# Performance work log

Measured on AMD Instinct MI355X. Metric: run time of the kernel, lower is better.

Reference implementation:

```python
import jax, jax.numpy as jnp
import numpy as np

NUM_HEADS = 8
ROPE_BASE = 10000.0


def _rope_cache(T, D, dtype=jnp.float32):
    # LLaMA-style rope cache: cos/sin of shape [T, D]
    inv_freq = 1.0 / (ROPE_BASE ** (jnp.arange(0, D, 2, dtype=dtype) / D))
    t = jnp.arange(T, dtype=dtype)
    freqs = t[:, None] * inv_freq[None, :]            # [T, D/2]
    emb = jnp.concatenate([freqs, freqs], axis=-1)    # [T, D]
    return jnp.cos(emb), jnp.sin(emb)


def _rotate_half(x):
    x1, x2 = jnp.split(x, 2, axis=-1)
    return jnp.concatenate([-x2, x1], axis=-1)


def setup_inputs() -> dict:
    key = jax.random.key(0)
    k1, k2, k3 = jax.random.split(key, 3)
    B, T, C = 4, 2048, 512
    x = jax.random.normal(k1, (B, T, C), dtype=jnp.float32)
    Wqkv = jax.random.normal(k2, (C, 3 * C), dtype=jnp.float32) * (1.0 / np.sqrt(C))
    Wproj = jax.random.normal(k3, (C, C), dtype=jnp.float32) * (1.0 / np.sqrt(C))
    return {"x": x, "Wqkv": Wqkv, "Wproj": Wproj}


def reference(x, Wqkv, Wproj):
    B, T, C = x.shape
    H = NUM_HEADS
    D = C // H

    qkv = jnp.einsum('btc,cf->btf', x, Wqkv)          # [B,T,3C]
    qkv = qkv.reshape(B, T, H, 3 * D)
    q, k, v = jnp.split(qkv, 3, axis=-1)              # each [B,T,H,D]
    q = q.transpose(0, 2, 1, 3)                       # [B,H,T,D]
    k = k.transpose(0, 2, 1, 3)
    v = v.transpose(0, 2, 1, 3)

    cos, sin = _rope_cache(T, D, dtype=x.dtype)       # [T,D]
    cos = cos[None, None, :, :]
    sin = sin[None, None, :, :]
    q = q * cos + _rotate_half(q) * sin
    k = k * cos + _rotate_half(k) * sin

    scale = 1.0 / np.sqrt(D)
    scores = jnp.einsum('bhqd,bhkd->bhqk', q, k) * scale  # [B,H,T,T]
    causal = jnp.tril(jnp.ones((T, T), dtype=bool))
    scores = jnp.where(causal[None, None, :, :], scores, jnp.finfo(scores.dtype).min)
    attn = jax.nn.softmax(scores, axis=-1)
    out = jnp.einsum('bhqk,bhkd->bhqd', attn, v)      # [B,H,T,D]
    out = out.transpose(0, 2, 1, 3).reshape(B, T, C)
    return jnp.einsum('btc,cd->btd', out, Wproj)
```

## Files before the change

### kernel.cpp

```cpp
#include <hip/hip_runtime.h>
#include <hip/hip_bf16.h>
#include <stdint.h>

constexpr int Bn = 4;
constexpr int Tn = 2048;
constexpr int Cn = 512;
constexpr int Hn = 8;
constexpr int Dn = 64;
constexpr int BT = Bn * Tn;
constexpr int NQKV = 3 * Cn;

typedef __attribute__((ext_vector_type(4))) float  f32x4;
typedef __attribute__((ext_vector_type(8))) short  s16x8;
typedef __attribute__((ext_vector_type(4))) short  s16x4;

__device__ __forceinline__ short f2bs(float f) {
    __hip_bfloat16 h = __float2bfloat16(f);
    return *reinterpret_cast<short*>(&h);
}

__device__ __forceinline__ void gload16(const short* g, short* l) {
    __builtin_amdgcn_global_load_lds(
        (const __attribute__((address_space(1))) void*)g,
        (__attribute__((address_space(3))) void*)l, 16, 0, 0);
}


__global__ __launch_bounds__(256) void k_prep(const float* __restrict__ x,
                                              const float* __restrict__ Wqkv,
                                              const float* __restrict__ Wproj,
                                              short* __restrict__ xb,
                                              short* __restrict__ wqkvT,
                                              short* __restrict__ wprojT,
                                              float2* __restrict__ csT) {
    const int bid = blockIdx.x;
    const int tid = threadIdx.x;
    __shared__ float lds[64 * 65];

    if (bid < 4096) {
        int i = bid * 256 + tid;
        f32x4 v = reinterpret_cast<const f32x4*>(x)[i];
        s16x4 o;
        o[0] = f2bs(v[0]); o[1] = f2bs(v[1]); o[2] = f2bs(v[2]); o[3] = f2bs(v[3]);
        reinterpret_cast<s16x4*>(xb)[i] = o;
    } else if (bid < 4352) {
        int wb = bid - 4096;
        const float* W; short* out; int N, n0, k0;
        if (wb < 192) {
            W = Wqkv; out = wqkvT; N = NQKV;
            n0 = (wb >> 3) * 64; k0 = (wb & 7) * 64;
        } else {
            wb -= 192;
            W = Wproj; out = wprojT; N = Cn;
            n0 = (wb >> 3) * 64; k0 = (wb & 7) * 64;
        }
#pragma unroll
        for (int i = 0; i < 16; ++i) {
            int flat = i * 256 + tid;
            int k = flat >> 6, n = flat & 63;
            lds[n * 65 + k] = W[(size_t)(k0 + k) * N + n0 + n];
        }
        __syncthreads();
#pragma unroll
        for (int i = 0; i < 16; ++i) {
            int flat = i * 256 + tid;
            int n = flat >> 6, k = flat & 63;
            out[(size_t)(n0 + n) * 512 + k0 + k] = f2bs(lds[n * 65 + k]);
        }
    } else {
        int i = (bid - 4352) * 256 + tid;
        int t = i >> 6, d = i & 63;
        float inv = exp2f(-(float)(d & 31) * 0.41524101186f);
        float fr = (float)t * inv;
        csT[i] = make_float2(cosf(fr), sinf(fr));
    }
}


template <int MODE>
__global__ __launch_bounds__(256, 4) void gemm_kernel(
    const short* __restrict__ A, const short* __restrict__ Bt,
    const float2* __restrict__ csT,
    short* __restrict__ Qb, short* __restrict__ Kb, short* __restrict__ Vt,
    float* __restrict__ outF) {
    const int m0 = blockIdx.y * 128;
    const int n0 = blockIdx.x * 128;
    const int tid = threadIdx.x;
    const int w = tid >> 6, lane = tid & 63;
    const int qi = lane & 15, g = lane >> 4;
    const int wr = w >> 1, wc = w & 1;

    __shared__ short As[2][128 * 32];
    __shared__ short Bs[2][128 * 32];

    f32x4 acc[4][4];
#pragma unroll
    for (int mt = 0; mt < 4; ++mt)
#pragma unroll
        for (int nt = 0; nt < 4; ++nt) acc[mt][nt] = (f32x4){0.f, 0.f, 0.f, 0.f};

    const int lrr = lane >> 2;
    const int lp = lane & 3;

#define STAGEG(buf, k0)                                                         \
    {                                                                           \
        _Pragma("unroll")                                                       \
        for (int i_ = 0; i_ < 2; ++i_) {                                        \
            int row_ = i_ * 64 + w * 16 + lrr;                                  \
            int c_ = lp ^ ((row_ ^ (row_ >> 2)) & 3);                           \
            gload16(&A[(size_t)(m0 + row_) * 512 + (k0) + c_ * 8],              \
                    &As[buf][(i_ * 64 + w * 16) * 32 + lane * 8]);              \
            gload16(&Bt[(size_t)(n0 + row_) * 512 + (k0) + c_ * 8],             \
                    &Bs[buf][(i_ * 64 + w * 16) * 32 + lane * 8]);              \
        }                                                                       \
    }

    STAGEG(0, 0);

    for (int it = 0; it < 16; ++it) {
        const int cur = it & 1;
        if (it + 1 < 16) {
            STAGEG((it + 1) & 1, (it + 1) * 32);
            asm volatile("s_waitcnt vmcnt(4)" ::: "memory");
        } else {
            asm volatile("s_waitcnt vmcnt(0)" ::: "memory");
        }
        __builtin_amdgcn_s_barrier();
        asm volatile("" ::: "memory");

        s16x8 af[4], bf[4];
#pragma unroll
        for (int mt = 0; mt < 4; ++mt) {
            int row = wr * 64 + mt * 16 + qi;
            int p = g ^ ((row ^ (row >> 2)) & 3);
            af[mt] = *(const s16x8*)&As[cur][row * 32 + p * 8];
        }
#pragma unroll
        for (int nt = 0; nt < 4; ++nt) {
            int row = wc * 64 + nt * 16 + qi;
            int p = g ^ ((row ^ (row >> 2)) & 3);
            bf[nt] = *(const s16x8*)&Bs[cur][row * 32 + p * 8];
        }
#pragma unroll
        for (int mt = 0; mt < 4; ++mt)
#pragma unroll
            for (int nt = 0; nt < 4; ++nt)
                acc[mt][nt] = __builtin_amdgcn_mfma_f32_16x16x32_bf16(
                    af[mt], bf[nt], acc[mt][nt], 0, 0, 0);

        asm volatile("" ::: "memory");
        __builtin_amdgcn_s_barrier();
        asm volatile("" ::: "memory");
    }
#undef STAGEG

    if (MODE == 1) {
#pragma unroll
        for (int mt = 0; mt < 4; ++mt)
#pragma unroll
            for (int nt = 0; nt < 4; ++nt)
#pragma unroll
                for (int r = 0; r < 4; ++r)
                    outF[(size_t)(m0 + wr * 64 + mt * 16 + 4 * g + r) * 512 +
                         n0 + wc * 64 + nt * 16 + qi] = acc[mt][nt][r];
    } else {
        const int seg64 = (n0 >> 6) + wc;
        const int h = seg64 / 3;
        const int seg = seg64 % 3;
        const int b = m0 >> 11;
        const int tb = (m0 & 2047) + wr * 64;
        const float QSC = 0.125f * 1.44269504f;
        if (seg == 2) {
            const size_t vbase = (size_t)(b * Hn + h) * Dn;
#pragma unroll
            for (int mt = 0; mt < 4; ++mt)
#pragma unroll
                for (int nt = 0; nt < 4; ++nt)
#pragma unroll
                    for (int r = 0; r < 4; ++r) {
                        int t = tb + mt * 16 + 4 * g + r;
                        int d = nt * 16 + qi;
                        int o = t & 31;
                        int jj = (t & ~31) + ((o >> 2) & 3) * 8 + (o >> 4) * 4 + (o & 3);
                        Vt[(vbase + d) * Tn + jj] = f2bs(acc[mt][nt][r]);
                    }
        } else {
            short* dst = (seg == 0) ? Qb : Kb;
            const float post = (seg == 0) ? QSC : 1.0f;
            const size_t headbase = (size_t)(b * Hn + h) * Tn;
#pragma unroll
            for (int mt = 0; mt < 4; ++mt)
#pragma unroll
                for (int nt = 0; nt < 4; ++nt)
#pragma unroll
                    for (int r = 0; r < 4; ++r) {
                        int t = tb + mt * 16 + 4 * g + r;
                        int d = nt * 16 + qi;
                        float val = acc[mt][nt][r];
                        float pv = (nt < 2) ? -acc[mt][nt + 2][r] : acc[mt][nt - 2][r];
                        float2 cs = csT[t * 64 + d];
                        dst[(headbase + t) * Dn + d] = f2bs((val * cs.x + pv * cs.y) * post);
                    }
        }
    }
}


__global__ __launch_bounds__(512, 4) void attn_kernel(const short* __restrict__ Qb,
                                                      const short* __restrict__ Kb,
                                                      const short* __restrict__ Vt,
                                                      short* __restrict__ AO) {
    const int idx = blockIdx.x;
    const int bh = idx & 31;
    const int qt = 31 - (idx >> 5);
    const int q0 = qt * 64;
    const int tid = threadIdx.x;
    const int w = tid >> 6, lane = tid & 63;
    const int qi = lane & 15, g = lane >> 4;
    const int grp = w >> 2;
    const int wg = w & 3;
    const int b = bh >> 3, h = bh & 7;

    __shared__ short Ks[2][2][64 * 64];
    __shared__ short Vs[2][2][64 * 64];

    const short* Qh = Qb + (size_t)bh * Tn * Dn;
    const short* Kh = Kb + (size_t)bh * Tn * Dn;
    const short* Vh = Vt + (size_t)bh * Dn * Tn;

    const int wrow0 = q0 + wg * 16;
    s16x8 qf[2];
#pragma unroll
    for (int dh = 0; dh < 2; ++dh)
        qf[dh] = *(const s16x8*)&Qh[(size_t)(wrow0 + qi) * Dn + dh * 32 + g * 8];

    f32x4 O[4];
#pragma unroll
    for (int dt = 0; dt < 4; ++dt) O[dt] = (f32x4){0.f, 0.f, 0.f, 0.f};
    float lsum = 0.f;

    const int nch = qt + 1;
    const int mid = (nch + 1) >> 1;
    const int chbase = grp ? mid : 0;
    const int nmy = grp ? (nch - mid) : mid;
    const f32x4 z4 = {0.f, 0.f, 0.f, 0.f};

    const int lr = lane >> 3;
    const int lc = (lane & 7) ^ lr;

#define STAGE(buf, ch)                                                          \
    {                                                                           \
        const int kv0_ = (ch) * 64;                                             \
        _Pragma("unroll")                                                       \
        for (int i_ = 0; i_ < 2; ++i_) {                                        \
            int slot_ = i_ * 4 + wg;                                            \
            int r_ = slot_ * 8 + lr;                                            \
            gload16(&Kh[(size_t)(kv0_ + r_) * 64 + lc * 8],                     \
                    &Ks[grp][buf][slot_ * 512 + lane * 8]);                     \
            gload16(&Vh[(size_t)r_ * Tn + kv0_ + lc * 8],                       \
                    &Vs[grp][buf][slot_ * 512 + lane * 8]);                     \
        }                                                                       \
    }

    if (nmy > 0) STAGE(0, chbase);

    for (int i = 0; i < mid; ++i) {
        const bool valid = i < nmy;
        const int ch = chbase + i;
        const int kv0 = ch * 64;
        const int cur = i & 1;
        if (valid) {
            if (i + 1 < nmy) {
                STAGE((i + 1) & 1, ch + 1);
                asm volatile("s_waitcnt vmcnt(4)" ::: "memory");
            } else {
                asm volatile("s_waitcnt vmcnt(0)" ::: "memory");
            }
        }
        __builtin_amdgcn_s_barrier();
        asm volatile("" ::: "memory");

        if (valid) {
            f32x4 sacc[4];
            __builtin_amdgcn_s_setprio(1);
#pragma unroll
            for (int sub = 0; sub < 4; ++sub) {
                const int krow = sub * 16 + qi;
                s16x8 ka = *(const s16x8*)&Ks[grp][cur][krow * 64 + ((g ^ (qi & 7))) * 8];
                s16x8 kc = *(const s16x8*)&Ks[grp][cur][krow * 64 + (((4 | g) ^ (qi & 7))) * 8];
                f32x4 t0 = __builtin_amdgcn_mfma_f32_16x16x32_bf16(ka, qf[0], z4, 0, 0, 0);
                sacc[sub] = __builtin_amdgcn_mfma_f32_16x16x32_bf16(kc, qf[1], t0, 0, 0, 0);
            }
            __builtin_amdgcn_s_setprio(0);

            float pe[16];
            if (kv0 + 63 <= wrow0) {
#pragma unroll
                for (int e2 = 0; e2 < 16; ++e2)
                    pe[e2] = exp2f(sacc[e2 >> 2][e2 & 3]);
            } else {
                const int qrow = wrow0 + qi;
#pragma unroll
                for (int sub = 0; sub < 4; ++sub)
#pragma unroll
                    for (int r = 0; r < 4; ++r) {
                        int key = kv0 + sub * 16 + 4 * g + r;
                        pe[sub * 4 + r] = (key <= qrow) ? exp2f(sacc[sub][r]) : 0.f;
                    }
            }
            {
                float a0 = (pe[0] + pe[1]) + (pe[2] + pe[3]);
                float a1 = (pe[4] + pe[5]) + (pe[6] + pe[7]);
                float a2 = (pe[8] + pe[9]) + (pe[10] + pe[11]);
                float a3 = (pe[12] + pe[13]) + (pe[14] + pe[15]);
                lsum += (a0 + a1) + (a2 + a3);
            }
            s16x8 pf[2];
#pragma unroll
            for (int c = 0; c < 2; ++c)
#pragma unroll
                for (int e2 = 0; e2 < 8; ++e2) pf[c][e2] = f2bs(pe[c * 8 + e2]);

            __builtin_amdgcn_s_setprio(1);
#pragma unroll
            for (int c = 0; c < 2; ++c)
#pragma unroll
                for (int dt = 0; dt < 4; ++dt) {
                    const int vrow = dt * 16 + qi;
                    s16x8 vf = *(const s16x8*)&Vs[grp][cur][vrow * 64 +
                                                   ((((c << 2) | g) ^ (qi & 7))) * 8];
                    O[dt] = __builtin_amdgcn_mfma_f32_16x16x32_bf16(
                        pf[c], vf, O[dt], 0, 0, 0);
                }
            __builtin_amdgcn_s_setprio(0);
        }
        asm volatile("" ::: "memory");
        __builtin_amdgcn_s_barrier();
        asm volatile("" ::: "memory");
    }
#undef STAGE

    lsum += __shfl_xor(lsum, 16);
    lsum += __shfl_xor(lsum, 32);

    f32x4* Osc = (f32x4*)&Ks[0][0][0];
    float* Lsc = (float*)&Vs[0][0][0];
    __syncthreads();
    if (grp == 1) {
#pragma unroll
        for (int dt = 0; dt < 4; ++dt)
            Osc[(dt * 4 + wg) * 64 + lane] = O[dt];
        if (g == 0) Lsc[wg * 16 + qi] = lsum;
    }
    __syncthreads();
    if (grp == 0) {
        float lt = lsum + Lsc[wg * 16 + qi];
#pragma unroll
        for (int dt = 0; dt < 4; ++dt) {
            f32x4 p = Osc[(dt * 4 + wg) * 64 + lane];
            O[dt][0] += p[0]; O[dt][1] += p[1]; O[dt][2] += p[2]; O[dt][3] += p[3];
        }
#pragma unroll
        for (int r = 0; r < 4; ++r) {
            float li = __shfl(lt, 4 * g + r);
            float inv = 1.f / li;
            int t = wrow0 + 4 * g + r;
#pragma unroll
            for (int dt = 0; dt < 4; ++dt)
                AO[((size_t)(b * Tn + t)) * Cn + h * 64 + dt * 16 + qi] =
                    f2bs(O[dt][r] * inv);
        }
    }
}


extern "C" void kernel_launch(void* const* d_in, const int* in_sizes, int n_in,
                              void* d_out, int out_size, void* d_ws, size_t ws_size,
                              hipStream_t stream) {
    const float* x = (const float*)d_in[0];
    const float* Wqkv = (const float*)d_in[1];
    const float* Wproj = (const float*)d_in[2];
    float* out = (float*)d_out;

    char* ws = (char*)d_ws;
    size_t o = 0;
    short* xb = (short*)(ws + o);      o += (size_t)BT * Cn * 2;
    short* wqkvT = (short*)(ws + o);   o += (size_t)NQKV * Cn * 2;
    short* wprojT = (short*)(ws + o);  o += (size_t)Cn * Cn * 2;
    short* Qb = (short*)(ws + o);      o += (size_t)Bn * Hn * Tn * Dn * 2;
    short* Kb = (short*)(ws + o);      o += (size_t)Bn * Hn * Tn * Dn * 2;
    short* Vt = (short*)(ws + o);      o += (size_t)Bn * Hn * Tn * Dn * 2;
    float2* csT = (float2*)(ws + o);   o += (size_t)Tn * Dn * 8;

    k_prep<<<dim3(4864), 256, 0, stream>>>(x, Wqkv, Wproj, xb, wqkvT, wprojT, csT);

    gemm_kernel<0><<<dim3(NQKV / 128, BT / 128), 256, 0, stream>>>(
        xb, wqkvT, csT, Qb, Kb, Vt, nullptr);

    attn_kernel<<<dim3(1024), 512, 0, stream>>>(Qb, Kb, Vt, xb );

    gemm_kernel<1><<<dim3(Cn / 128, BT / 128), 256, 0, stream>>>(
        xb , wprojT, csT, nullptr, nullptr, nullptr, out);
}
```

Baseline: 80.87 us.

## Shrink attention KV chunks to 32 keys and raise occupancy

The KV chunk size in the attention kernel drops from 64 to 32 keys. Two wave groups still split the causal range, each now taking exactly qt+1 chunks, so the idle-iteration imbalance disappears. LDS per block is halved and launch bounds go from 4 to 8 blocks per CU, with a new XOR swizzle for the narrower V tile. This brings more barriers and iterations per key, each with less MFMA work between them, in exchange for higher occupancy and better load balance.

```diff
diff --git a/kernel.cpp b/kernel.cpp
--- a/kernel.cpp
+++ b/kernel.cpp
@@ -206,7 +206,7 @@
 }
 
 
-__global__ __launch_bounds__(512, 4) void attn_kernel(const short* __restrict__ Qb,
+__global__ __launch_bounds__(512, 8) void attn_kernel(const short* __restrict__ Qb,
                                                       const short* __restrict__ Kb,
                                                       const short* __restrict__ Vt,
                                                       short* __restrict__ AO) {
@@ -221,8 +221,8 @@
     const int wg = w & 3;
     const int b = bh >> 3, h = bh & 7;
 
-    __shared__ short Ks[2][2][64 * 64];
-    __shared__ short Vs[2][2][64 * 64];
+    __shared__ short Ks[2][2][32 * 64];
+    __shared__ short Vs[2][2][64 * 32];
 
     const short* Qh = Qb + (size_t)bh * Tn * Dn;
     const short* Kh = Kb + (size_t)bh * Tn * Dn;
@@ -239,101 +239,85 @@
     for (int dt = 0; dt < 4; ++dt) O[dt] = (f32x4){0.f, 0.f, 0.f, 0.f};
     float lsum = 0.f;
 
-    const int nch = qt + 1;
-    const int mid = (nch + 1) >> 1;
+    const int mid = qt + 1;
     const int chbase = grp ? mid : 0;
-    const int nmy = grp ? (nch - mid) : mid;
     const f32x4 z4 = {0.f, 0.f, 0.f, 0.f};
 
-    const int lr = lane >> 3;
-    const int lc = (lane & 7) ^ lr;
-
-#define STAGE(buf, ch)                                                          \
-    {                                                                           \
-        const int kv0_ = (ch) * 64;                                             \
-        _Pragma("unroll")                                                       \
-        for (int i_ = 0; i_ < 2; ++i_) {                                        \
-            int slot_ = i_ * 4 + wg;                                            \
-            int r_ = slot_ * 8 + lr;                                            \
-            gload16(&Kh[(size_t)(kv0_ + r_) * 64 + lc * 8],                     \
-                    &Ks[grp][buf][slot_ * 512 + lane * 8]);                     \
-            gload16(&Vh[(size_t)r_ * Tn + kv0_ + lc * 8],                       \
-                    &Vs[grp][buf][slot_ * 512 + lane * 8]);                     \
-        }                                                                       \
-    }
-
-    if (nmy > 0) STAGE(0, chbase);
+    const int klr = lane >> 3;
+    const int klc = (lane & 7) ^ klr;
+    const int vdr = wg * 16 + (lane >> 2);
+    const int vvc = (lane & 3) ^ ((vdr ^ (vdr >> 2)) & 3);
+
+#define STAGE(buf, ch)                                                         \
+    {                                                                          \
+        const int kv0_ = (ch) * 32;                                            \
+        gload16(&Kh[(size_t)(kv0_ + wg * 8 + klr) * 64 + klc * 8],             \
+                &Ks[grp][buf][wg * 512 + lane * 8]);                           \
+        gload16(&Vh[(size_t)vdr * Tn + kv0_ + vvc * 8],                        \
+                &Vs[grp][buf][wg * 512 + lane * 8]);                           \
+    }
+
+    STAGE(0, chbase);
 
     for (int i = 0; i < mid; ++i) {
-        const bool valid = i < nmy;
         const int ch = chbase + i;
-        const int kv0 = ch * 64;
+        const int kv0 = ch * 32;
         const int cur = i & 1;
-        if (valid) {
-            if (i + 1 < nmy) {
-                STAGE((i + 1) & 1, ch + 1);
-                asm volatile("s_waitcnt vmcnt(4)" ::: "memory");
-            } else {
-                asm volatile("s_waitcnt vmcnt(0)" ::: "memory");
-            }
+        if (i + 1 < mid) {
+            STAGE((i + 1) & 1, ch + 1);
+            asm volatile("s_waitcnt vmcnt(2)" ::: "memory");
+        } else {
+            asm volatile("s_waitcnt vmcnt(0)" ::: "memory");
         }
         __builtin_amdgcn_s_barrier();
         asm volatile("" ::: "memory");
 
-        if (valid) {
-            f32x4 sacc[4];
-            __builtin_amdgcn_s_setprio(1);
-#pragma unroll
-            for (int sub = 0; sub < 4; ++sub) {
-                const int krow = sub * 16 + qi;
-                s16x8 ka = *(const s16x8*)&Ks[grp][cur][krow * 64 + ((g ^ (qi & 7))) * 8];
-                s16x8 kc = *(const s16x8*)&Ks[grp][cur][krow * 64 + (((4 | g) ^ (qi & 7))) * 8];
-                f32x4 t0 = __builtin_amdgcn_mfma_f32_16x16x32_bf16(ka, qf[0], z4, 0, 0, 0);
-                sacc[sub] = __builtin_amdgcn_mfma_f32_16x16x32_bf16(kc, qf[1], t0, 0, 0, 0);
-            }
-            __builtin_amdgcn_s_setprio(0);
-
-            float pe[16];
-            if (kv0 + 63 <= wrow0) {
-#pragma unroll
-                for (int e2 = 0; e2 < 16; ++e2)
-                    pe[e2] = exp2f(sacc[e2 >> 2][e2 & 3]);
-            } else {
-                const int qrow = wrow0 + qi;
-#pragma unroll
-                for (int sub = 0; sub < 4; ++sub)
-#pragma unroll
-                    for (int r = 0; r < 4; ++r) {
-                        int key = kv0 + sub * 16 + 4 * g + r;
-                        pe[sub * 4 + r] = (key <= qrow) ? exp2f(sacc[sub][r]) : 0.f;
-                    }
-            }
-            {
-                float a0 = (pe[0] + pe[1]) + (pe[2] + pe[3]);
-                float a1 = (pe[4] + pe[5]) + (pe[6] + pe[7]);
-                float a2 = (pe[8] + pe[9]) + (pe[10] + pe[11]);
-                float a3 = (pe[12] + pe[13]) + (pe[14] + pe[15]);
-                lsum += (a0 + a1) + (a2 + a3);
-            }
-            s16x8 pf[2];
-#pragma unroll
-            for (int c = 0; c < 2; ++c)
-#pragma unroll
-                for (int e2 = 0; e2 < 8; ++e2) pf[c][e2] = f2bs(pe[c * 8 + e2]);
-
-            __builtin_amdgcn_s_setprio(1);
-#pragma unroll
-            for (int c = 0; c < 2; ++c)
-#pragma unroll
-                for (int dt = 0; dt < 4; ++dt) {
-                    const int vrow = dt * 16 + qi;
-                    s16x8 vf = *(const s16x8*)&Vs[grp][cur][vrow * 64 +
-                                                   ((((c << 2) | g) ^ (qi & 7))) * 8];
-                    O[dt] = __builtin_amdgcn_mfma_f32_16x16x32_bf16(
-                        pf[c], vf, O[dt], 0, 0, 0);
+        f32x4 sacc[2];
+        __builtin_amdgcn_s_setprio(1);
+#pragma unroll
+        for (int sub = 0; sub < 2; ++sub) {
+            const int krow = sub * 16 + qi;
+            s16x8 ka = *(const s16x8*)&Ks[grp][cur][krow * 64 + ((g ^ (qi & 7))) * 8];
+            s16x8 kc = *(const s16x8*)&Ks[grp][cur][krow * 64 + (((4 | g) ^ (qi & 7))) * 8];
+            f32x4 t0 = __builtin_amdgcn_mfma_f32_16x16x32_bf16(ka, qf[0], z4, 0, 0, 0);
+            sacc[sub] = __builtin_amdgcn_mfma_f32_16x16x32_bf16(kc, qf[1], t0, 0, 0, 0);
+        }
+        __builtin_amdgcn_s_setprio(0);
+
+        float pe[8];
+        if (kv0 + 31 <= wrow0) {
+#pragma unroll
+            for (int e2 = 0; e2 < 8; ++e2)
+                pe[e2] = exp2f(sacc[e2 >> 2][e2 & 3]);
+        } else {
+            const int qrow = wrow0 + qi;
+#pragma unroll
+            for (int sub = 0; sub < 2; ++sub)
+#pragma unroll
+                for (int r = 0; r < 4; ++r) {
+                    int key = kv0 + sub * 16 + 4 * g + r;
+                    pe[sub * 4 + r] = (key <= qrow) ? exp2f(sacc[sub][r]) : 0.f;
                 }
-            __builtin_amdgcn_s_setprio(0);
-        }
+        }
+        {
+            float a0 = (pe[0] + pe[1]) + (pe[2] + pe[3]);
+            float a1 = (pe[4] + pe[5]) + (pe[6] + pe[7]);
+            lsum += a0 + a1;
+        }
+        s16x8 pf;
+#pragma unroll
+        for (int e2 = 0; e2 < 8; ++e2) pf[e2] = f2bs(pe[e2]);
+
+        __builtin_amdgcn_s_setprio(1);
+#pragma unroll
+        for (int dt = 0; dt < 4; ++dt) {
+            const int vrow = dt * 16 + qi;
+            s16x8 vf = *(const s16x8*)&Vs[grp][cur][vrow * 32 +
+                                           ((g ^ ((vrow ^ (vrow >> 2)) & 3))) * 8];
+            O[dt] = __builtin_amdgcn_mfma_f32_16x16x32_bf16(pf, vf, O[dt], 0, 0, 0);
+        }
+        __builtin_amdgcn_s_setprio(0);
+
         asm volatile("" ::: "memory");
         __builtin_amdgcn_s_barrier();
         asm volatile("" ::: "memory");
```

After: 82.92 us. +2.5%, slower.
